# Optimization experiments

Hardware: AMD Instinct MI355X
Metric: run time of the kernel (lower is better)

Reference implementation:

```python
import jax, jax.numpy as jnp
import numpy as np
import math

B_, H_, W_ = 2, 32, 32
DM, DS = 192, 16
RK = math.ceil(DM / 16)  # dt_rank 'auto'
DI = 2 * DM              # d_inner = expand_factor * d_model


def setup_inputs() -> dict:
    key = jax.random.key(0)
    ks = jax.random.split(key, 8)
    x = jax.random.normal(ks[0], (B_, H_, W_, DM), jnp.float32)
    W_in = jax.random.normal(ks[1], (DM, DI), jnp.float32) * 0.02
    b_in = jnp.zeros((DI,), jnp.float32)
    W_x = jax.random.normal(ks[2], (DI, 2 * RK + 2 * DS), jnp.float32) * 0.02
    b_x = jnp.zeros((2 * RK + 2 * DS,), jnp.float32)
    std = RK ** -0.5
    W_dtT = jax.random.uniform(ks[3], (RK, DI), jnp.float32, -std, std)
    W_dtL = jax.random.uniform(ks[4], (RK, DI), jnp.float32, -std, std)
    # dt bias init exactly as in the torch module
    dt = jnp.exp(jax.random.uniform(ks[5], (DI,), jnp.float32)
                 * (math.log(0.1) - math.log(0.001)) + math.log(0.001))
    dt = jnp.clip(dt, 1e-4)
    inv_dt = dt + jnp.log(-jnp.expm1(-dt))
    A = jnp.tile(jnp.arange(1, DS + 1, dtype=jnp.float32), (DI, 1))
    AT_log = jnp.log(A)
    AL_log = jnp.log(A)
    D = jnp.ones((DI,), jnp.float32)
    W_out = jax.random.normal(ks[6], (DI, DM), jnp.float32) * 0.02
    b_out = jnp.zeros((DM,), jnp.float32)
    return dict(x=x, W_in=W_in, b_in=b_in, W_x=W_x, b_x=b_x,
                W_dtT=W_dtT, b_dtT=inv_dt, W_dtL=W_dtL, b_dtL=inv_dt,
                AT_log=AT_log, AL_log=AL_log, D=D, W_out=W_out, b_out=b_out)


def _wavefront_scan(dAT, dAL, bx):
    """2D wavefront linear recurrence over an (H, W) grid.
    h[i,j] = 0.5*dAT[i,j]*h[i-1,j] + 0.5*dAL[i,j]*h[i,j-1] + bx[i,j]
    Inputs: (B, H, W, d_inner, d_state). Sequential over rows (lax.scan),
    parallel linear recurrence along columns (associative_scan)."""
    def combine(c1, c2):
        a1, u1 = c1
        a2, u2 = c2
        return a2 * a1, a2 * u1 + u2

    def row_step(h_prev, row):
        dAT_r, dAL_r, bx_r = row                     # (B, W, di, ds)
        u = 0.5 * dAT_r * h_prev + bx_r              # top contribution folded in
        a = 0.5 * dAL_r
        _, h = jax.lax.associative_scan(combine, (a, u), axis=1)
        return h, h

    rows = (jnp.moveaxis(dAT, 1, 0), jnp.moveaxis(dAL, 1, 0), jnp.moveaxis(bx, 1, 0))
    h0 = jnp.zeros(dAT.shape[:1] + dAT.shape[2:], dAT.dtype)
    _, hs = jax.lax.scan(row_step, h0, rows)         # (H, B, W, di, ds)
    return jnp.moveaxis(hs, 0, 1)                    # (B, H, W, di, ds)


def reference(x, W_in, b_in, W_x, b_x, W_dtT, b_dtT, W_dtL, b_dtL,
              AT_log, AL_log, D, W_out, b_out):
    # in_proj + GELU (torch nn.GELU default = exact erf)
    h = jax.nn.gelu(x @ W_in + b_in, approximate=False)   # (B,H,W,DI)
    # proj_and_discretise
    dbc = h @ W_x + b_x
    dT, dL, Bm, Cm = jnp.split(dbc, [RK, 2 * RK, 2 * RK + DS], axis=-1)
    deltaT = jax.nn.softplus(dT @ W_dtT + b_dtT)          # (B,H,W,DI)
    deltaL = jax.nn.softplus(dL @ W_dtL + b_dtL)
    AT = -jnp.exp(AT_log)                                  # (DI,DS)
    AL = -jnp.exp(AL_log)
    dAT = jnp.exp(deltaT[..., None] * AT)                  # (B,H,W,DI,DS)
    dAL = jnp.exp(deltaL[..., None] * AL)
    BXT = (deltaT * h)[..., None] * Bm[..., None, :]       # delta*B*x
    BXL = (deltaL * h)[..., None] * Bm[..., None, :]
    # 2D wavefront selective scan
    hs = _wavefront_scan(dAT, dAL, 0.5 * (BXT + BXL))
    y = jnp.einsum('bhwds,bhws->bhwd', hs, Cm) + h * D
    # act2 + out_proj
    y = jax.nn.gelu(y, approximate=False)
    return y @ W_out + b_out
```

## Files before the change

kernel.cpp:

```cpp
#include <hip/hip_runtime.h>
#include <math.h>

#define TOK 2048
#define DMOD 192
#define DI 384
#define DS 16
#define RK 12
#define NCOL 56
#define HH 32
#define WW 32
#define BB 2

__device__ __forceinline__ float gelu_exact(float x) {
    return 0.5f * x * (1.0f + erff(x * 0.70710678118654752f));
}
__device__ __forceinline__ float softplus_f(float x) {
    return (x > 20.0f) ? x : log1pf(expf(x));
}
__device__ __forceinline__ float bperm(int byte_addr, float v) {
    return __uint_as_float((unsigned)__builtin_amdgcn_ds_bpermute(
        byte_addr, (int)__float_as_uint(v)));
}

__global__ __launch_bounds__(128) void K_h(
        const float* __restrict__ x, const float* __restrict__ W_in,
        const float* __restrict__ b_in, float* __restrict__ h_tm,
        float* __restrict__ ht) {
    __shared__ float xs[4 * DMOD];
    int tx = threadIdx.x;
    int n = blockIdx.x * 128 + tx;
    int tok0 = blockIdx.y * 4;
    const float* xg = x + (long)tok0 * DMOD;
#pragma unroll
    for (int q = 0; q < 6; ++q) xs[q * 128 + tx] = xg[q * 128 + tx];
    __syncthreads();
    float acc[4];
    float bi = b_in[n];
#pragma unroll
    for (int t = 0; t < 4; ++t) acc[t] = bi;
#pragma unroll 2
    for (int k = 0; k < DMOD; k += 4) {
        float w0 = W_in[(k + 0) * DI + n];
        float w1 = W_in[(k + 1) * DI + n];
        float w2 = W_in[(k + 2) * DI + n];
        float w3 = W_in[(k + 3) * DI + n];
#pragma unroll
        for (int t = 0; t < 4; ++t) {
            float4 xv = *(const float4*)&xs[t * DMOD + k];
            acc[t] = fmaf(xv.x, w0, acc[t]);
            acc[t] = fmaf(xv.y, w1, acc[t]);
            acc[t] = fmaf(xv.z, w2, acc[t]);
            acc[t] = fmaf(xv.w, w3, acc[t]);
        }
    }
    float hv[4];
#pragma unroll
    for (int t = 0; t < 4; ++t) {
        hv[t] = gelu_exact(acc[t]);
        h_tm[(long)(tok0 + t) * DI + n] = hv[t];
    }
    int b = tok0 >> 10, ij = tok0 & 1023;
    *(float4*)&ht[(long)(b * DI + n) * 1024 + ij] =
        make_float4(hv[0], hv[1], hv[2], hv[3]);
}

__global__ __launch_bounds__(128) void K_dbc(
        const float* __restrict__ h_tm, const float* __restrict__ W_x,
        const float* __restrict__ b_x, float* __restrict__ dbcT) {
    int tid = threadIdx.x;
    int c = tid & 63;
    int ce = (c < NCOL) ? c : 0;
    int mA = __builtin_amdgcn_readfirstlane(blockIdx.x * 4 + (tid >> 6) * 2);
    const float* hA = h_tm + (long)mA * DI;
    const float* hB = hA + DI;
    const float* Wp = W_x + ce;
    float a0 = 0.f, a1 = 0.f, b0 = 0.f, b1 = 0.f;
#pragma unroll 2
    for (int k = 0; k < DI; k += 4) {
        float w0 = Wp[(k + 0) * NCOL], w1 = Wp[(k + 1) * NCOL];
        float w2 = Wp[(k + 2) * NCOL], w3 = Wp[(k + 3) * NCOL];
        a0 = fmaf(hA[k + 0], w0, a0);  a1 = fmaf(hA[k + 1], w1, a1);
        a0 = fmaf(hA[k + 2], w2, a0);  a1 = fmaf(hA[k + 3], w3, a1);
        b0 = fmaf(hB[k + 0], w0, b0);  b1 = fmaf(hB[k + 1], w1, b1);
        b0 = fmaf(hB[k + 2], w2, b0);  b1 = fmaf(hB[k + 3], w3, b1);
    }
    if (c < NCOL) {
        float bx = b_x[c];
        int b = mA >> 10, ij = mA & 1023;
        long o = (long)(b * NCOL + c) * 1024 + ij;
        dbcT[o]     = a0 + a1 + bx;
        dbcT[o + 1] = b0 + b1 + bx;
    }
}

__global__ __launch_bounds__(256) void k3_scan(
        const float* __restrict__ ht, const float* __restrict__ dbcT,
        const float* __restrict__ W_dtT, const float* __restrict__ b_dtT,
        const float* __restrict__ W_dtL, const float* __restrict__ b_dtL,
        const float* __restrict__ AT_log, const float* __restrict__ AL_log,
        const float* __restrict__ Dv, float* __restrict__ yt) {
    __shared__ float part[8][HH][WW];
    __shared__ float ldT[1024];
    __shared__ float ldL[1024];
    int bd = blockIdx.x;
    int b = bd / DI, d = bd - b * DI;
    int tid = threadIdx.x;
    const float* db = dbcT + (long)b * NCOL * 1024;

    {
        float wTr[RK], wLr[RK];
#pragma unroll
        for (int r = 0; r < RK; ++r) {
            wTr[r] = W_dtT[r * DI + d];
            wLr[r] = W_dtL[r * DI + d];
        }
        float bT = b_dtT[d], bL = b_dtL[d];
#pragma unroll
        for (int q = 0; q < 4; ++q) {
            int cell = q * 256 + tid;
            float aT = bT, aL = bL;
#pragma unroll
            for (int r = 0; r < RK; ++r) {
                aT = fmaf(db[(long)r * 1024 + cell],        wTr[r], aT);
                aL = fmaf(db[(long)(RK + r) * 1024 + cell], wLr[r], aL);
            }
            ldT[cell] = softplus_f(aT);
            ldL[cell] = softplus_f(aL);
        }
    }
    __syncthreads();

    int w = tid >> 6, lane = tid & 63;
    int s1 = lane >> 5, j = lane & 31;
    int p = w * 2 + s1;

    float AT0 = -__expf(AT_log[d * DS + 2 * p]);
    float AT1 = -__expf(AT_log[d * DS + 2 * p + 1]);
    float AL0 = -__expf(AL_log[d * DS + 2 * p]);
    float AL1 = -__expf(AL_log[d * DS + 2 * p + 1]);

    const float* hr  = ht + (long)bd * 1024;
    const float* B0r = db + (long)(24 + 2 * p) * 1024;
    const float* B1r = B0r + 1024;
    const float* C0r = db + (long)(40 + 2 * p) * 1024;
    const float* C1r = C0r + 1024;

    int ba1  = ((j >= 1  ? lane - 1  : lane) << 2);
    int ba2  = ((j >= 2  ? lane - 2  : lane) << 2);
    int ba4  = ((j >= 4  ? lane - 4  : lane) << 2);
    int ba8  = ((j >= 8  ? lane - 8  : lane) << 2);
    int ba16 = ((j >= 16 ? lane - 16 : lane) << 2);

    float hp0 = 0.f, hp1 = 0.f;
    float nh = hr[j];
    float nB0 = B0r[j], nB1 = B1r[j], nC0 = C0r[j], nC1 = C1r[j];

#pragma unroll 1
    for (int i = 0; i < HH; ++i) {
        float chv = nh;
        float cB0 = nB0, cB1 = nB1, cC0 = nC0, cC1 = nC1;
        int nx = (i + 1 < HH) ? (i + 1) * 32 + j : j;
        nh = hr[nx];
        nB0 = B0r[nx]; nB1 = B1r[nx]; nC0 = C0r[nx]; nC1 = C1r[nx];

        float cT = ldT[i * 32 + j];
        float cL = ldL[i * 32 + j];
        float g  = 0.5f * (cT + cL) * chv;
        float a0 = 0.5f * __expf(cL * AL0);
        float a1 = 0.5f * __expf(cL * AL1);
        float u0 = fmaf(0.5f * __expf(cT * AT0), hp0, g * cB0);
        float u1 = fmaf(0.5f * __expf(cT * AT1), hp1, g * cB1);

#define SCAN_STEP(BA, OFF)                                            \
        {                                                             \
            float au0 = bperm(BA, a0), uu0 = bperm(BA, u0);           \
            float au1 = bperm(BA, a1), uu1 = bperm(BA, u1);           \
            bool m = (j >= OFF);                                      \
            uu0 = m ? uu0 : 0.f;  au0 = m ? au0 : 1.f;                \
            uu1 = m ? uu1 : 0.f;  au1 = m ? au1 : 1.f;                \
            u0 = fmaf(a0, uu0, u0);  a0 *= au0;                       \
            u1 = fmaf(a1, uu1, u1);  a1 *= au1;                       \
        }
        SCAN_STEP(ba1, 1)  SCAN_STEP(ba2, 2)  SCAN_STEP(ba4, 4)
        SCAN_STEP(ba8, 8)  SCAN_STEP(ba16, 16)
#undef SCAN_STEP

        hp0 = u0;  hp1 = u1;
        part[p][i][j] = fmaf(u0, cC0, u1 * cC1);
    }
    __syncthreads();

    float Dd = Dv[d];
    float* yr = yt + (long)bd * 1024;
    const float* pf = &part[0][0][0];
#pragma unroll
    for (int q = 0; q < 4; ++q) {
        int cell = q * 256 + tid;
        float sum = pf[cell]           + pf[1024 + cell] +
                    pf[2 * 1024 + cell] + pf[3 * 1024 + cell] +
                    pf[4 * 1024 + cell] + pf[5 * 1024 + cell] +
                    pf[6 * 1024 + cell] + pf[7 * 1024 + cell];
        yr[cell] = gelu_exact(sum + hr[cell] * Dd);
    }
}

__global__ __launch_bounds__(DMOD) void K_out(
        const float* __restrict__ yt, const float* __restrict__ W_out,
        const float* __restrict__ b_out, float* __restrict__ out) {
    int n = threadIdx.x;
    int tok0 = blockIdx.x * 4;
    int b = tok0 >> 10;
    const float* yb = yt + (long)b * DI * 1024 + (tok0 & 1023);
    float acc[4];
    float bo = b_out[n];
#pragma unroll
    for (int t = 0; t < 4; ++t) acc[t] = bo;
#pragma unroll 2
    for (int dd = 0; dd < DI; ++dd) {
        float w = W_out[dd * DMOD + n];
        float4 y4 = *(const float4*)(yb + (long)dd * 1024);
        acc[0] = fmaf(y4.x, w, acc[0]);
        acc[1] = fmaf(y4.y, w, acc[1]);
        acc[2] = fmaf(y4.z, w, acc[2]);
        acc[3] = fmaf(y4.w, w, acc[3]);
    }
#pragma unroll
    for (int t = 0; t < 4; ++t)
        out[(long)(tok0 + t) * DMOD + n] = acc[t];
}

extern "C" void kernel_launch(void* const* d_in, const int* in_sizes, int n_in,
                              void* d_out, int out_size, void* d_ws, size_t ws_size,
                              hipStream_t stream) {
    const float* x      = (const float*)d_in[0];
    const float* W_in   = (const float*)d_in[1];
    const float* b_in   = (const float*)d_in[2];
    const float* W_x    = (const float*)d_in[3];
    const float* b_x    = (const float*)d_in[4];
    const float* W_dtT  = (const float*)d_in[5];
    const float* b_dtT  = (const float*)d_in[6];
    const float* W_dtL  = (const float*)d_in[7];
    const float* b_dtL  = (const float*)d_in[8];
    const float* AT_log = (const float*)d_in[9];
    const float* AL_log = (const float*)d_in[10];
    const float* Dv     = (const float*)d_in[11];
    const float* W_out  = (const float*)d_in[12];
    const float* b_out  = (const float*)d_in[13];
    float* out = (float*)d_out;

    float* ws = (float*)d_ws;
    const long NE = (long)BB * DI * 1024;
    float* h_tm = ws;
    float* ht   = ws + NE;
    float* dbcT = ws + 2 * NE;
    float* yt   = ht;

    K_h  <<<dim3(3, TOK / 4), 128, 0, stream>>>(x, W_in, b_in, h_tm, ht);
    K_dbc<<<TOK / 4, 128, 0, stream>>>(h_tm, W_x, b_x, dbcT);
    k3_scan<<<BB * DI, 256, 0, stream>>>(ht, dbcT,
                                         W_dtT, b_dtT, W_dtL, b_dtL,
                                         AT_log, AL_log, Dv, yt);
    K_out<<<TOK / 4, DMOD, 0, stream>>>(yt, W_out, b_out, out);
}
```

Baseline: 197.5 us.

## Use DPP row shifts for column scan and retile output projection

Swaps the ds_bpermute-based Hillis-Steele scan across 32 columns for DPP row_shr moves with bound-control defaults, plus a row_bcast15 step to cross 16-lane rows. This removes the LDS-permute latency and the select masking on every scan step. K_out is also restructured: each 64-thread block now owns 64 tokens and 6 output channels, so y reads are coalesced per lane and W_out values are wave-uniform broadcasts. The broadcast step relies on DPP row_bcast semantics being correct for 32-lane halves, and the new K_out tiling changes the grid shape and how much data is reused.

```diff
diff --git a/kernel.cpp b/kernel.cpp
--- a/kernel.cpp
+++ b/kernel.cpp
@@ -17,9 +17,10 @@
 __device__ __forceinline__ float softplus_f(float x) {
     return (x > 20.0f) ? x : log1pf(expf(x));
 }
-__device__ __forceinline__ float bperm(int byte_addr, float v) {
-    return __uint_as_float((unsigned)__builtin_amdgcn_ds_bpermute(
-        byte_addr, (int)__float_as_uint(v)));
+template<int CTRL, int ROW_MASK>
+__device__ __forceinline__ float dpp_mov(float old_v, float src) {
+    return __int_as_float(__builtin_amdgcn_update_dpp(
+        __float_as_int(old_v), __float_as_int(src), CTRL, ROW_MASK, 0xF, false));
 }
 
 __global__ __launch_bounds__(128) void K_h(
@@ -145,12 +146,6 @@
     const float* C0r = db + (long)(40 + 2 * p) * 1024;
     const float* C1r = C0r + 1024;
 
-    int ba1  = ((j >= 1  ? lane - 1  : lane) << 2);
-    int ba2  = ((j >= 2  ? lane - 2  : lane) << 2);
-    int ba4  = ((j >= 4  ? lane - 4  : lane) << 2);
-    int ba8  = ((j >= 8  ? lane - 8  : lane) << 2);
-    int ba16 = ((j >= 16 ? lane - 16 : lane) << 2);
-
     float hp0 = 0.f, hp1 = 0.f;
     float nh = hr[j];
     float nB0 = B0r[j], nB1 = B1r[j], nC0 = C0r[j], nC1 = C1r[j];
@@ -171,19 +166,26 @@
         float u0 = fmaf(0.5f * __expf(cT * AT0), hp0, g * cB0);
         float u1 = fmaf(0.5f * __expf(cT * AT1), hp1, g * cB1);
 
-#define SCAN_STEP(BA, OFF)                                            \
+#define DPP_STEP(CTRL)                                                \
         {                                                             \
-            float au0 = bperm(BA, a0), uu0 = bperm(BA, u0);           \
-            float au1 = bperm(BA, a1), uu1 = bperm(BA, u1);           \
-            bool m = (j >= OFF);                                      \
-            uu0 = m ? uu0 : 0.f;  au0 = m ? au0 : 1.f;                \
-            uu1 = m ? uu1 : 0.f;  au1 = m ? au1 : 1.f;                \
+            float uu0 = dpp_mov<CTRL, 0xF>(0.0f, u0);                 \
+            float au0 = dpp_mov<CTRL, 0xF>(1.0f, a0);                 \
+            float uu1 = dpp_mov<CTRL, 0xF>(0.0f, u1);                 \
+            float au1 = dpp_mov<CTRL, 0xF>(1.0f, a1);                 \
             u0 = fmaf(a0, uu0, u0);  a0 *= au0;                       \
             u1 = fmaf(a1, uu1, u1);  a1 *= au1;                       \
         }
-        SCAN_STEP(ba1, 1)  SCAN_STEP(ba2, 2)  SCAN_STEP(ba4, 4)
-        SCAN_STEP(ba8, 8)  SCAN_STEP(ba16, 16)
-#undef SCAN_STEP
+        DPP_STEP(0x111)
+        DPP_STEP(0x112)
+        DPP_STEP(0x114)
+        DPP_STEP(0x118)
+#undef DPP_STEP
+        {
+            float ub0 = dpp_mov<0x142, 0xA>(0.0f, u0);
+            float ub1 = dpp_mov<0x142, 0xA>(0.0f, u1);
+            u0 = fmaf(a0, ub0, u0);
+            u1 = fmaf(a1, ub1, u1);
+        }
 
         hp0 = u0;  hp1 = u1;
         part[p][i][j] = fmaf(u0, cC0, u1 * cC1);
@@ -204,29 +206,38 @@
     }
 }
 
-__global__ __launch_bounds__(DMOD) void K_out(
+__global__ __launch_bounds__(64) void K_out(
         const float* __restrict__ yt, const float* __restrict__ W_out,
         const float* __restrict__ b_out, float* __restrict__ out) {
-    int n = threadIdx.x;
-    int tok0 = blockIdx.x * 4;
-    int b = tok0 >> 10;
-    const float* yb = yt + (long)b * DI * 1024 + (tok0 & 1023);
-    float acc[4];
-    float bo = b_out[n];
-#pragma unroll
-    for (int t = 0; t < 4; ++t) acc[t] = bo;
-#pragma unroll 2
-    for (int dd = 0; dd < DI; ++dd) {
-        float w = W_out[dd * DMOD + n];
-        float4 y4 = *(const float4*)(yb + (long)dd * 1024);
-        acc[0] = fmaf(y4.x, w, acc[0]);
-        acc[1] = fmaf(y4.y, w, acc[1]);
-        acc[2] = fmaf(y4.z, w, acc[2]);
-        acc[3] = fmaf(y4.w, w, acc[3]);
-    }
-#pragma unroll
-    for (int t = 0; t < 4; ++t)
-        out[(long)(tok0 + t) * DMOD + n] = acc[t];
+    int lane = threadIdx.x;
+    int tok_tile = blockIdx.x >> 5;
+    int nch = blockIdx.x & 31;
+    int n0 = nch * 6;
+    int tok0 = tok_tile * 64;
+    int b = tok0 >> 10, ij0 = tok0 & 1023;
+    const float* yb = yt + (long)b * DI * 1024 + ij0 + lane;
+
+    float acc[6];
+#pragma unroll
+    for (int q = 0; q < 6; ++q) acc[q] = b_out[n0 + q];
+
+#pragma unroll 1
+    for (int d = 0; d < DI; d += 8) {
+        float yv[8];
+#pragma unroll
+        for (int u = 0; u < 8; ++u)
+            yv[u] = yb[(long)(d + u) * 1024];
+#pragma unroll
+        for (int u = 0; u < 8; ++u) {
+            const float* wr = W_out + (long)(d + u) * DMOD + n0;
+#pragma unroll
+            for (int q = 0; q < 6; ++q)
+                acc[q] = fmaf(yv[u], wr[q], acc[q]);
+        }
+    }
+    float* op = out + (long)(tok0 + lane) * DMOD + n0;
+#pragma unroll
+    for (int q = 0; q < 6; ++q) op[q] = acc[q];
 }
 
 extern "C" void kernel_launch(void* const* d_in, const int* in_sizes, int n_in,
@@ -260,5 +271,5 @@
     k3_scan<<<BB * DI, 256, 0, stream>>>(ht, dbcT,
                                          W_dtT, b_dtT, W_dtL, b_dtL,
                                          AT_log, AL_log, Dv, yt);
-    K_out<<<TOK / 4, DMOD, 0, stream>>>(yt, W_out, b_out, out);
-}
+    K_out<<<32 * 32, 64, 0, stream>>>(yt, W_out, b_out, out);
+}
```

New measurement: 181.3 us. 1.09x faster.
